# Performance work log

Measured on AMD Instinct MI355X. Metric: run time of the kernel, lower is better.

The kernel has to match this reference:

```python
import jax, jax.numpy as jnp
import numpy as np

B, S, D, H = 1, 4096, 768, 12
Dh = D // H  # 64


def setup_inputs() -> dict:
    key = jax.random.key(0)
    ks = jax.random.split(key, 11)
    w = lambda k, sh: jax.random.normal(k, sh, jnp.float32) * 0.02
    return {
        "query": jax.random.normal(ks[0], (B, S, D), jnp.float32),
        "key": jax.random.normal(ks[1], (B, S, D), jnp.float32),
        "value": jax.random.normal(ks[2], (B, S, D), jnp.float32),
        "mask": jnp.ones((B, S), jnp.int32),  # nonzero = attend; mask==0 positions are filled with -inf
        "Wq": w(ks[3], (D, D)), "bq": w(ks[4], (D,)),
        "Wk": w(ks[5], (D, D)), "bk": w(ks[6], (D,)),
        "Wv": w(ks[7], (D, D)), "bv": w(ks[8], (D,)),
        "Wo": w(ks[9], (D, D)), "bo": w(ks[10], (D,)),
    }


def reference(query, key, value, mask, Wq, bq, Wk, bk, Wv, bv, Wo, bo):
    # shape(): (B, S, D) -> (B, H, S, Dh)
    def split_heads(x):
        return x.reshape(B, S, H, Dh).transpose(0, 2, 1, 3)

    q = split_heads(query @ Wq.T + bq) / np.sqrt(Dh).astype(np.float32)
    k = split_heads(key @ Wk.T + bk)
    # multi_rand_attn_cuda is an unbiased randomized estimator of
    # weights @ v_lin(value); the exact-math baseline applies v_lin then
    # contracts with the attention weights per head.
    v = split_heads(value @ Wv.T + bv)

    scores = jnp.einsum('bhqd,bhkd->bhqk', q, k)  # (B,H,S,S)
    scores = jnp.where((mask == 0)[:, None, None, :], -jnp.inf, scores)
    weights = jax.nn.softmax(scores, axis=-1)  # dropout is identity at eval

    ctx = jnp.einsum('bhqk,bhkd->bhqd', weights, v)
    ctx = ctx.transpose(0, 2, 1, 3).reshape(B, S, D)  # unshape
    return ctx @ Wo.T + bo
```

## Files before the change

### kernel.cpp

```cpp
#include <hip/hip_runtime.h>

#define S_LEN 4096
#define D_MODEL 768
#define N_HEADS 12
#define D_HEAD 64

typedef short bf16x8 __attribute__((ext_vector_type(8)));
typedef float f32x4 __attribute__((ext_vector_type(4)));
typedef float f32x16 __attribute__((ext_vector_type(16)));
typedef float f32x4v __attribute__((ext_vector_type(4)));
typedef unsigned short u16;
typedef unsigned short u16x8 __attribute__((ext_vector_type(8)));
typedef unsigned int u32;

__device__ __forceinline__ u16 f2bf(float f) {
  unsigned u = __float_as_uint(f);
  u += 0x7FFFu + ((u >> 16) & 1u);
  return (u16)(u >> 16);
}

__device__ __forceinline__ u32 pk2bf(float lo, float hi) {
  u32 a = __float_as_uint(hi) + 0x8000u;
  u32 b = __float_as_uint(lo) + 0x8000u;
  return __builtin_amdgcn_perm(a, b, 0x07060302u);
}

__device__ __forceinline__ void gl_lds16(const void* g, void* l) {
  __builtin_amdgcn_global_load_lds(
      (const __attribute__((address_space(1))) void*)g,
      (__attribute__((address_space(3))) void*)l, 16, 0, 0);
}

struct CvtArgs {
  const float* s[4];
  u16* d[4];
};

__global__ __launch_bounds__(256) void cvt8_kernel(CvtArgs a, long n) {
  const float* s = a.s[blockIdx.z];
  u16* d = a.d[blockIdx.z];
  long i = ((long)blockIdx.x * 256 + threadIdx.x) * 8;
  if (i >= n) return;
  f32x4v v0 = *(const f32x4v*)(s + i);
  f32x4v v1 = *(const f32x4v*)(s + i + 4);
  u16x8 o;
#pragma unroll
  for (int j = 0; j < 4; ++j) { o[j] = f2bf(v0[j]); o[j + 4] = f2bf(v1[j]); }
  *(u16x8*)(d + i) = o;
}

struct ProjArgs {
  const u16* A[3];
  const u16* W[3];
  const float* bias[3];
  void* out[3];
  float scale[3];
  int mode[3];
};

template <int TM>
__global__ __launch_bounds__(256, TM == 128 ? 2 : 4) void proj_kernel(ProjArgs args) {
  constexpr int MF = TM / 32;
  constexpr int CA = TM / 16;
  const int z = blockIdx.z;
  const u16* __restrict__ A = args.A[z];
  const u16* __restrict__ W = args.W[z];
  const float* __restrict__ bias = args.bias[z];
  const float scale = args.scale[z];
  const int mode = args.mode[z];

  __shared__ u16 Al[TM * 32];
  __shared__ u16 Bl[128 * 32];

  const int tid = threadIdx.x;
  const int w = tid >> 6, l = tid & 63;
  const int l15 = l & 15, quad = l >> 4;
  const int m0 = blockIdx.x * TM;
  const int n0 = blockIdx.y * 128;
  const int wm = (w & 1) * (TM / 2), wn = (w >> 1) * 64;
  const int crow = l >> 2, ccol = (l & 3) * 8;

  f32x4 acc[MF][4] = {};

  for (int kt = 0; kt < 24; ++kt) {
    const int k0 = kt * 32;
#pragma unroll
    for (int i = 0; i < CA / 4; ++i) {
      const int sub = w * (CA / 4) + i;
      const int row = sub * 16 + crow;
      gl_lds16(&A[(size_t)(m0 + row) * D_MODEL + k0 + ccol], &Al[sub * 512 + l * 8]);
    }
#pragma unroll
    for (int i = 0; i < 2; ++i) {
      const int sub = w * 2 + i;
      const int row = sub * 16 + crow;
      gl_lds16(&W[(size_t)(n0 + row) * D_MODEL + k0 + ccol], &Bl[sub * 512 + l * 8]);
    }
    __syncthreads();
    bf16x8 af[MF], bfr[4];
#pragma unroll
    for (int mf = 0; mf < MF; ++mf)
      af[mf] = *(const bf16x8*)&Al[(wm + mf * 16 + l15) * 32 + quad * 8];
#pragma unroll
    for (int nf = 0; nf < 4; ++nf)
      bfr[nf] = *(const bf16x8*)&Bl[(wn + nf * 16 + l15) * 32 + quad * 8];
#pragma unroll
    for (int mf = 0; mf < MF; ++mf)
#pragma unroll
      for (int nf = 0; nf < 4; ++nf)
        acc[mf][nf] = __builtin_amdgcn_mfma_f32_16x16x32_bf16(af[mf], bfr[nf], acc[mf][nf], 0, 0, 0);
    __syncthreads();
  }

#pragma unroll
  for (int nf = 0; nf < 4; ++nf) {
    const int col = n0 + wn + nf * 16 + l15;
    const float bv = bias[col];
#pragma unroll
    for (int mf = 0; mf < MF; ++mf) {
#pragma unroll
      for (int r = 0; r < 4; ++r) {
        const int row = m0 + wm + mf * 16 + quad * 4 + r;
        const float v = (acc[mf][nf][r] + bv) * scale;
        if (mode == 0) {
          ((u16*)args.out[z])[(size_t)row * D_MODEL + col] = f2bf(v);
        } else if (mode == 2) {
          ((float*)args.out[z])[(size_t)row * D_MODEL + col] = v;
        } else if (mode == 3) {
          const int hh = col >> 6, d = col & 63;
          const int st = row >> 5, kl = row & 31;
          const int s = d >> 4, gg = (d >> 3) & 1, j = d & 7;
          ((u16*)args.out[z])[(size_t)((hh * 128 + st) * 4 + s) * 512 + (gg * 32 + kl) * 8 + j] = f2bf(v);
        } else {
          const int hh = col >> 6, d = col & 63;
          const int st = row >> 5, r16 = row & 15, u = (row >> 4) & 1;
          const int j = (r16 & 3) | (((r16 >> 3) & 1) << 2);
          const int gg = (r16 >> 2) & 1;
          const int db = (d >> 5) & 1, vl = d & 31;
          ((u16*)args.out[z])[(size_t)((hh * 128 + st) * 4 + db * 2 + u) * 512 + (gg * 32 + vl) * 8 + j] = f2bf(v);
        }
      }
    }
  }
}

__global__ __launch_bounds__(256, 2) void flash_kernel(
    const u16* __restrict__ Qb, const u16* __restrict__ Kpk,
    const u16* __restrict__ Vpk, const int* __restrict__ mask,
    u16* __restrict__ Ctx) {
  __shared__ char smem[67584];

  const int tid = threadIdx.x;
  const int w = tid >> 6, l = tid & 63;
  const int l31 = l & 31, g = l >> 5;
  const int h = blockIdx.y;
  const int q0 = blockIdx.x * 64;

  bf16x8 qf[2][4];
#pragma unroll
  for (int qs = 0; qs < 2; ++qs) {
    const u16* qrow = Qb + (size_t)(q0 + qs * 32 + l31) * D_MODEL + h * D_HEAD + g * 8;
#pragma unroll
    for (int s = 0; s < 4; ++s) qf[qs][s] = *(const bf16x8*)(qrow + s * 16);
  }

  const u16* kb = Kpk + ((size_t)h * 128 + w * 32) * 2048 + l * 8;
  const u16* vb = Vpk + ((size_t)h * 128 + w * 32) * 2048 + l * 8;
  const int* mk = mask + w * 1024 + l31;

  f32x16 oacc[2][2] = {};
  float lsum[2] = {0.f, 0.f};

  bf16x8 kfA[4], vfA[4], kfB[4], vfB[4];
  int mvA, mvB;

  mvA = mk[0];
#pragma unroll
  for (int c = 0; c < 4; ++c) kfA[c] = *(const bf16x8*)(kb + c * 512);
#pragma unroll
  for (int c = 0; c < 4; ++c) vfA[c] = *(const bf16x8*)(vb + c * 512);

#define FLASH_COMPUTE(KF, VF, MV)                                              \
  {                                                                            \
    const unsigned long long mb = __ballot((MV) != 0);                         \
    _Pragma("unroll") for (int qs = 0; qs < 2; ++qs) {                         \
      f32x16 sacc = {};                                                        \
      _Pragma("unroll") for (int s = 0; s < 4; ++s)                            \
          sacc = __builtin_amdgcn_mfma_f32_32x32x16_bf16(KF[s], qf[qs][s],     \
                                                         sacc, 0, 0, 0);       \
      _Pragma("unroll") for (int r = 0; r < 16; ++r)                           \
          sacc[r] = __builtin_amdgcn_exp2f(sacc[r]);                           \
      if (mb + 1ull != 0ull) {                                                 \
        const unsigned mh = (unsigned)(mb >> (4 * g));                         \
        _Pragma("unroll") for (int r = 0; r < 16; ++r)                         \
            if (!((mh >> ((r & 3) + 8 * (r >> 2))) & 1u)) sacc[r] = 0.f;       \
      }                                                                        \
      float ts = 0.f;                                                          \
      _Pragma("unroll") for (int r = 0; r < 16; ++r) ts += sacc[r];            \
      lsum[qs] += ts;                                                          \
      u32 pk[8];                                                               \
      _Pragma("unroll") for (int i = 0; i < 8; ++i)                            \
          pk[i] = pk2bf(sacc[2 * i], sacc[2 * i + 1]);                         \
      _Pragma("unroll") for (int u = 0; u < 2; ++u) {                          \
        union { u32 u4[4]; bf16x8 s; } bp;                                     \
        _Pragma("unroll") for (int i = 0; i < 4; ++i) bp.u4[i] = pk[4 * u + i];\
        oacc[qs][0] = __builtin_amdgcn_mfma_f32_32x32x16_bf16(VF[u], bp.s,     \
                                                              oacc[qs][0], 0, 0, 0); \
        oacc[qs][1] = __builtin_amdgcn_mfma_f32_32x32x16_bf16(VF[2 + u], bp.s, \
                                                              oacc[qs][1], 0, 0, 0); \
      }                                                                        \
    }                                                                          \
  }

  for (int p = 0; p < 16; ++p) {
    {
      const int nt = 2 * p + 1;
      mvB = mk[nt * 32];
      const u16* kn = kb + (size_t)nt * 2048;
      const u16* vn = vb + (size_t)nt * 2048;
#pragma unroll
      for (int c = 0; c < 4; ++c) kfB[c] = *(const bf16x8*)(kn + c * 512);
#pragma unroll
      for (int c = 0; c < 4; ++c) vfB[c] = *(const bf16x8*)(vn + c * 512);
      FLASH_COMPUTE(kfA, vfA, mvA)
    }
    {
      const int nt = (2 * p + 2 < 32) ? 2 * p + 2 : 31;
      mvA = mk[nt * 32];
      const u16* kn = kb + (size_t)nt * 2048;
      const u16* vn = vb + (size_t)nt * 2048;
#pragma unroll
      for (int c = 0; c < 4; ++c) kfA[c] = *(const bf16x8*)(kn + c * 512);
#pragma unroll
      for (int c = 0; c < 4; ++c) vfA[c] = *(const bf16x8*)(vn + c * 512);
      FLASH_COMPUTE(kfB, vfB, mvB)
    }
  }
#undef FLASH_COMPUTE

  float* Ol = (float*)smem;
  float* Ll = (float*)(smem + 65536);
#pragma unroll
  for (int qs = 0; qs < 2; ++qs) {
#pragma unroll
    for (int db = 0; db < 2; ++db)
#pragma unroll
      for (int r = 0; r < 16; ++r)
        Ol[((w * 4 + qs * 2 + db) * 16 + r) * 64 + l] = oacc[qs][db][r];
    Ll[w * 128 + qs * 64 + l] = lsum[qs];
  }
  __syncthreads();

  const int qs = w & 1, db = w >> 1;
  float Lt = 0.f;
#pragma unroll
  for (int kq = 0; kq < 4; ++kq)
    Lt += Ll[kq * 128 + qs * 64 + l] + Ll[kq * 128 + qs * 64 + (l ^ 32)];
  const float linv = 1.0f / Lt;
#pragma unroll
  for (int rr = 0; rr < 4; ++rr) {
    float v[4];
#pragma unroll
    for (int i = 0; i < 4; ++i) {
      const int r = rr * 4 + i;
      float acc = 0.f;
#pragma unroll
      for (int kq = 0; kq < 4; ++kq)
        acc += Ol[((kq * 4 + qs * 2 + db) * 16 + r) * 64 + l];
      v[i] = acc * linv;
    }
    u16* cp = Ctx + (size_t)(q0 + qs * 32 + l31) * D_MODEL + h * D_HEAD + db * 32 + rr * 8 + 4 * g;
    *(u32*)(cp) = pk2bf(v[0], v[1]);
    *(u32*)(cp + 2) = pk2bf(v[2], v[3]);
  }
}

extern "C" void kernel_launch(void* const* d_in, const int* in_sizes, int n_in,
                              void* d_out, int out_size, void* d_ws, size_t ws_size,
                              hipStream_t stream) {
  const float* query = (const float*)d_in[0];
  const float* key   = (const float*)d_in[1];
  const float* value = (const float*)d_in[2];
  const int*   maskp = (const int*)d_in[3];
  const float* Wq = (const float*)d_in[4];
  const float* bq = (const float*)d_in[5];
  const float* Wk = (const float*)d_in[6];
  const float* bk = (const float*)d_in[7];
  const float* Wv = (const float*)d_in[8];
  const float* bv = (const float*)d_in[9];
  const float* Wo = (const float*)d_in[10];
  const float* bo = (const float*)d_in[11];

  char* ws = (char*)d_ws;
  const size_t SZX = (size_t)S_LEN * D_MODEL * 2;
  const size_t SZW = (size_t)D_MODEL * D_MODEL * 2;
  u16* Xq  = (u16*)(ws);
  u16* Xk  = (u16*)(ws + SZX);
  u16* Xv  = (u16*)(ws + 2 * SZX);
  u16* Qb  = (u16*)(ws + 3 * SZX);
  u16* Kpk = (u16*)(ws + 4 * SZX);
  u16* Vpk = (u16*)(ws + 5 * SZX);
  u16* Wqb = (u16*)(ws + 6 * SZX);
  u16* Wkb = (u16*)(ws + 6 * SZX + SZW);
  u16* Wvb = (u16*)(ws + 6 * SZX + 2 * SZW);
  u16* Wob = (u16*)(ws + 6 * SZX + 3 * SZW);
  u16* Ctx = Xq;

  CvtArgs ca;
  ca.s[0] = query; ca.s[1] = key; ca.s[2] = value; ca.s[3] = query;
  ca.d[0] = Xq;    ca.d[1] = Xk;  ca.d[2] = Xv;    ca.d[3] = Xq;
  cvt8_kernel<<<dim3(1536, 1, 3), 256, 0, stream>>>(ca, (long)S_LEN * D_MODEL);

  CvtArgs cw;
  cw.s[0] = Wq;  cw.s[1] = Wk;  cw.s[2] = Wv;  cw.s[3] = Wo;
  cw.d[0] = Wqb; cw.d[1] = Wkb; cw.d[2] = Wvb; cw.d[3] = Wob;
  cvt8_kernel<<<dim3(288, 1, 4), 256, 0, stream>>>(cw, (long)D_MODEL * D_MODEL);

  ProjArgs pa;
  pa.A[0] = Xq;  pa.A[1] = Xk;  pa.A[2] = Xv;
  pa.W[0] = Wqb; pa.W[1] = Wkb; pa.W[2] = Wvb;
  pa.bias[0] = bq; pa.bias[1] = bk; pa.bias[2] = bv;
  pa.out[0] = Qb; pa.out[1] = Kpk; pa.out[2] = Vpk;
  pa.scale[0] = 0.125f * 1.4426950408889634f; pa.scale[1] = 1.f; pa.scale[2] = 1.f;
  pa.mode[0] = 0; pa.mode[1] = 3; pa.mode[2] = 4;
  proj_kernel<64><<<dim3(64, 6, 3), 256, 0, stream>>>(pa);

  flash_kernel<<<dim3(64, N_HEADS, 1), 256, 0, stream>>>(Qb, Kpk, Vpk, maskp, Ctx);

  ProjArgs po;
  po.A[0] = Ctx; po.A[1] = Ctx; po.A[2] = Ctx;
  po.W[0] = Wob; po.W[1] = Wob; po.W[2] = Wob;
  po.bias[0] = bo; po.bias[1] = bo; po.bias[2] = bo;
  po.out[0] = d_out; po.out[1] = d_out; po.out[2] = d_out;
  po.scale[0] = 1.f; po.scale[1] = 1.f; po.scale[2] = 1.f;
  po.mode[0] = 2; po.mode[1] = 2; po.mode[2] = 2;
  proj_kernel<64><<<dim3(64, 6, 1), 256, 0, stream>>>(po);
}
```

Baseline: 220.6 us.

## Merge conversion launches, stage packed K/V epilogue in LDS, shrink flash LDS

Merges the two fp32-to-bf16 conversion launches into one seven-slice launch. The QKV projection moves to 128-row tiles and, for the packed K/V layouts, stages the output tile in shared memory so it can be written with 16-byte coalesced stores instead of scattered 2-byte stores. The flash kernel's final reduction now works on one query half at a time, roughly halving its shared memory so three blocks can fit per CU. The extra synchronisation and smaller projection grid may offset part of the benefit.

```diff
diff --git a/kernel.cpp b/kernel.cpp
--- a/kernel.cpp
+++ b/kernel.cpp
@@ -31,16 +31,18 @@
       (__attribute__((address_space(3))) void*)l, 16, 0, 0);
 }
 
-struct CvtArgs {
-  const float* s[4];
-  u16* d[4];
+struct CvtArgs7 {
+  const float* s[7];
+  u16* d[7];
+  long n[7];
 };
 
-__global__ __launch_bounds__(256) void cvt8_kernel(CvtArgs a, long n) {
-  const float* s = a.s[blockIdx.z];
-  u16* d = a.d[blockIdx.z];
+__global__ __launch_bounds__(256) void cvt8_kernel(CvtArgs7 a) {
+  const int z = blockIdx.z;
+  const float* s = a.s[z];
+  u16* d = a.d[z];
   long i = ((long)blockIdx.x * 256 + threadIdx.x) * 8;
-  if (i >= n) return;
+  if (i >= a.n[z]) return;
   f32x4v v0 = *(const f32x4v*)(s + i);
   f32x4v v1 = *(const f32x4v*)(s + i + 4);
   u16x8 o;
@@ -59,7 +61,7 @@
 };
 
 template <int TM>
-__global__ __launch_bounds__(256, TM == 128 ? 2 : 4) void proj_kernel(ProjArgs args) {
+__global__ __launch_bounds__(256, 2) void proj_kernel(ProjArgs args) {
   constexpr int MF = TM / 32;
   constexpr int CA = TM / 16;
   const int z = blockIdx.z;
@@ -71,6 +73,7 @@
 
   __shared__ u16 Al[TM * 32];
   __shared__ u16 Bl[128 * 32];
+  __shared__ u16 Ep[TM == 128 ? 16384 : 1];
 
   const int tid = threadIdx.x;
   const int w = tid >> 6, l = tid & 63;
@@ -112,43 +115,63 @@
     __syncthreads();
   }
 
-#pragma unroll
-  for (int nf = 0; nf < 4; ++nf) {
-    const int col = n0 + wn + nf * 16 + l15;
-    const float bv = bias[col];
-#pragma unroll
-    for (int mf = 0; mf < MF; ++mf) {
-#pragma unroll
-      for (int r = 0; r < 4; ++r) {
-        const int row = m0 + wm + mf * 16 + quad * 4 + r;
-        const float v = (acc[mf][nf][r] + bv) * scale;
-        if (mode == 0) {
-          ((u16*)args.out[z])[(size_t)row * D_MODEL + col] = f2bf(v);
-        } else if (mode == 2) {
-          ((float*)args.out[z])[(size_t)row * D_MODEL + col] = v;
-        } else if (mode == 3) {
-          const int hh = col >> 6, d = col & 63;
-          const int st = row >> 5, kl = row & 31;
-          const int s = d >> 4, gg = (d >> 3) & 1, j = d & 7;
-          ((u16*)args.out[z])[(size_t)((hh * 128 + st) * 4 + s) * 512 + (gg * 32 + kl) * 8 + j] = f2bf(v);
-        } else {
-          const int hh = col >> 6, d = col & 63;
-          const int st = row >> 5, r16 = row & 15, u = (row >> 4) & 1;
-          const int j = (r16 & 3) | (((r16 >> 3) & 1) << 2);
-          const int gg = (r16 >> 2) & 1;
-          const int db = (d >> 5) & 1, vl = d & 31;
-          ((u16*)args.out[z])[(size_t)((hh * 128 + st) * 4 + db * 2 + u) * 512 + (gg * 32 + vl) * 8 + j] = f2bf(v);
+  if (mode == 3 || mode == 4) {
+#pragma unroll
+    for (int nf = 0; nf < 4; ++nf) {
+      const float bv = bias[n0 + wn + nf * 16 + l15];
+#pragma unroll
+      for (int mf = 0; mf < MF; ++mf) {
+#pragma unroll
+        for (int r = 0; r < 4; ++r) {
+          const float v = acc[mf][nf][r] + bv;
+          int off;
+          if (mode == 3) {
+            off = (((w >> 1) * 16 + ((w & 1) * 2 + (mf >> 1)) * 4 + nf) << 9) +
+                  (((l15 >> 3) * 32 + (mf & 1) * 16 + quad * 4 + r) << 3) + (l15 & 7);
+          } else {
+            off = (((w >> 1) * 16 + ((w & 1) * 2 + (mf >> 1)) * 4 + (nf >> 1) * 2 + (mf & 1)) << 9) +
+                  (((quad & 1) * 32 + (nf & 1) * 16 + l15) << 3) + r + 4 * (quad >> 1);
+          }
+          Ep[off] = f2bf(v);
         }
       }
     }
-  }
-}
-
-__global__ __launch_bounds__(256, 2) void flash_kernel(
+    __syncthreads();
+    const int hh0 = n0 >> 6, st0 = m0 >> 5;
+    u16* outp = (u16*)args.out[z];
+#pragma unroll
+    for (int hloc = 0; hloc < 2; ++hloc) {
+      u16* dst = outp + ((size_t)((hh0 + hloc) * 128 + st0) * 4) * 512;
+#pragma unroll
+      for (int c = 0; c < 4; ++c) {
+        u16x8 v = *(u16x8*)&Ep[hloc * 8192 + w * 2048 + c * 512 + l * 8];
+        *(u16x8*)(dst + w * 2048 + c * 512 + l * 8) = v;
+      }
+    }
+  } else {
+#pragma unroll
+    for (int nf = 0; nf < 4; ++nf) {
+      const int col = n0 + wn + nf * 16 + l15;
+      const float bv = bias[col];
+#pragma unroll
+      for (int mf = 0; mf < MF; ++mf) {
+#pragma unroll
+        for (int r = 0; r < 4; ++r) {
+          const int row = m0 + wm + mf * 16 + quad * 4 + r;
+          const float v = (acc[mf][nf][r] + bv) * scale;
+          if (mode == 0) ((u16*)args.out[z])[(size_t)row * D_MODEL + col] = f2bf(v);
+          else           ((float*)args.out[z])[(size_t)row * D_MODEL + col] = v;
+        }
+      }
+    }
+  }
+}
+
+__global__ __launch_bounds__(256, 3) void flash_kernel(
     const u16* __restrict__ Qb, const u16* __restrict__ Kpk,
     const u16* __restrict__ Vpk, const int* __restrict__ mask,
     u16* __restrict__ Ctx) {
-  __shared__ char smem[67584];
+  __shared__ char smem[34816];
 
   const int tid = threadIdx.x;
   const int w = tid >> 6, l = tid & 63;
@@ -239,39 +262,43 @@
 #undef FLASH_COMPUTE
 
   float* Ol = (float*)smem;
-  float* Ll = (float*)(smem + 65536);
-#pragma unroll
-  for (int qs = 0; qs < 2; ++qs) {
+  float* Ll = (float*)(smem + 32768);
+  Ll[w * 128 + l] = lsum[0];
+  Ll[w * 128 + 64 + l] = lsum[1];
+#pragma unroll
+  for (int ph = 0; ph < 2; ++ph) {
+    __syncthreads();
 #pragma unroll
     for (int db = 0; db < 2; ++db)
 #pragma unroll
       for (int r = 0; r < 16; ++r)
-        Ol[((w * 4 + qs * 2 + db) * 16 + r) * 64 + l] = oacc[qs][db][r];
-    Ll[w * 128 + qs * 64 + l] = lsum[qs];
-  }
-  __syncthreads();
-
-  const int qs = w & 1, db = w >> 1;
-  float Lt = 0.f;
-#pragma unroll
-  for (int kq = 0; kq < 4; ++kq)
-    Lt += Ll[kq * 128 + qs * 64 + l] + Ll[kq * 128 + qs * 64 + (l ^ 32)];
-  const float linv = 1.0f / Lt;
-#pragma unroll
-  for (int rr = 0; rr < 4; ++rr) {
-    float v[4];
-#pragma unroll
-    for (int i = 0; i < 4; ++i) {
-      const int r = rr * 4 + i;
-      float acc = 0.f;
-#pragma unroll
-      for (int kq = 0; kq < 4; ++kq)
-        acc += Ol[((kq * 4 + qs * 2 + db) * 16 + r) * 64 + l];
-      v[i] = acc * linv;
-    }
-    u16* cp = Ctx + (size_t)(q0 + qs * 32 + l31) * D_MODEL + h * D_HEAD + db * 32 + rr * 8 + 4 * g;
-    *(u32*)(cp) = pk2bf(v[0], v[1]);
-    *(u32*)(cp + 2) = pk2bf(v[2], v[3]);
+        Ol[((w * 2 + db) * 16 + r) * 64 + l] = oacc[ph][db][r];
+    __syncthreads();
+
+    float Lt = 0.f;
+#pragma unroll
+    for (int kq = 0; kq < 4; ++kq)
+      Lt += Ll[kq * 128 + ph * 64 + l] + Ll[kq * 128 + ph * 64 + (l ^ 32)];
+    const float linv = 1.0f / Lt;
+
+    const int db = w & 1;
+#pragma unroll
+    for (int t = 0; t < 2; ++t) {
+      const int rr = (w >> 1) * 2 + t;
+      float v[4];
+#pragma unroll
+      for (int i = 0; i < 4; ++i) {
+        const int r = rr * 4 + i;
+        float acc = 0.f;
+#pragma unroll
+        for (int kq = 0; kq < 4; ++kq)
+          acc += Ol[((kq * 2 + db) * 16 + r) * 64 + l];
+        v[i] = acc * linv;
+      }
+      u16* cp = Ctx + (size_t)(q0 + ph * 32 + l31) * D_MODEL + h * D_HEAD + db * 32 + rr * 8 + 4 * g;
+      *(u32*)(cp) = pk2bf(v[0], v[1]);
+      *(u32*)(cp + 2) = pk2bf(v[2], v[3]);
+    }
   }
 }
 
@@ -306,15 +333,15 @@
   u16* Wob = (u16*)(ws + 6 * SZX + 3 * SZW);
   u16* Ctx = Xq;
 
-  CvtArgs ca;
-  ca.s[0] = query; ca.s[1] = key; ca.s[2] = value; ca.s[3] = query;
-  ca.d[0] = Xq;    ca.d[1] = Xk;  ca.d[2] = Xv;    ca.d[3] = Xq;
-  cvt8_kernel<<<dim3(1536, 1, 3), 256, 0, stream>>>(ca, (long)S_LEN * D_MODEL);
-
-  CvtArgs cw;
-  cw.s[0] = Wq;  cw.s[1] = Wk;  cw.s[2] = Wv;  cw.s[3] = Wo;
-  cw.d[0] = Wqb; cw.d[1] = Wkb; cw.d[2] = Wvb; cw.d[3] = Wob;
-  cvt8_kernel<<<dim3(288, 1, 4), 256, 0, stream>>>(cw, (long)D_MODEL * D_MODEL);
+  CvtArgs7 cc;
+  cc.s[0] = query; cc.s[1] = key; cc.s[2] = value;
+  cc.s[3] = Wq; cc.s[4] = Wk; cc.s[5] = Wv; cc.s[6] = Wo;
+  cc.d[0] = Xq; cc.d[1] = Xk; cc.d[2] = Xv;
+  cc.d[3] = Wqb; cc.d[4] = Wkb; cc.d[5] = Wvb; cc.d[6] = Wob;
+  const long nact = (long)S_LEN * D_MODEL, nw = (long)D_MODEL * D_MODEL;
+  cc.n[0] = cc.n[1] = cc.n[2] = nact;
+  cc.n[3] = cc.n[4] = cc.n[5] = cc.n[6] = nw;
+  cvt8_kernel<<<dim3(1536, 1, 7), 256, 0, stream>>>(cc);
 
   ProjArgs pa;
   pa.A[0] = Xq;  pa.A[1] = Xk;  pa.A[2] = Xv;
@@ -323,7 +350,7 @@
   pa.out[0] = Qb; pa.out[1] = Kpk; pa.out[2] = Vpk;
   pa.scale[0] = 0.125f * 1.4426950408889634f; pa.scale[1] = 1.f; pa.scale[2] = 1.f;
   pa.mode[0] = 0; pa.mode[1] = 3; pa.mode[2] = 4;
-  proj_kernel<64><<<dim3(64, 6, 3), 256, 0, stream>>>(pa);
+  proj_kernel<128><<<dim3(32, 6, 3), 256, 0, stream>>>(pa);
 
   flash_kernel<<<dim3(64, N_HEADS, 1), 256, 0, stream>>>(Qb, Kpk, Vpk, maskp, Ctx);
 
```

After: 350.1 us. 1.59x slower.
